# Optimization experiments

Measured on AMD Instinct MI355X. Metric: run time of the kernel, lower is better.

The kernel has to match this reference:

```python
import jax, jax.numpy as jnp
import numpy as np

B, S, D, H = 32, 512, 640, 10
DK = D // H           # 64
NUM_ITER = 3          # capsule routing iterations


def _proj(x, W, b):
    # [B,S,D] @ [D,D]^T -> split heads -> [B,H,S,DK]
    b_, s_, _ = x.shape
    return (x @ W.T + b).reshape(b_, s_, H, DK).transpose(0, 2, 1, 3)


def _squash(t, eps=1e-9):
    sn = jnp.sum(t * t, axis=-1, keepdims=True)
    return (sn / (1.0 + sn)) * t / jnp.sqrt(sn + eps)


def setup_inputs() -> dict:
    key0 = jax.random.key(0)
    ks = jax.random.split(key0, 12)
    s = 1.0 / np.sqrt(D)
    return {
        "query": jax.random.normal(ks[0], (B, S, D), jnp.float32),
        "key": jax.random.normal(ks[1], (B, S, D), jnp.float32),
        "value": jax.random.normal(ks[2], (B, S, D), jnp.float32),
        "mask": jax.random.randint(ks[3], (B, 1, S, S), 0, 2, jnp.int32),
        "adj": jax.random.uniform(ks[4], (B, S, S), jnp.float32),
        "layer": 2,
        "Wq": jax.random.normal(ks[5], (D, D), jnp.float32) * s,
        "bq": jnp.zeros((D,), jnp.float32),
        "Wk": jax.random.normal(ks[6], (D, D), jnp.float32) * s,
        "bk": jnp.zeros((D,), jnp.float32),
        "Wv": jax.random.normal(ks[7], (D, D), jnp.float32) * s,
        "bv": jnp.zeros((D,), jnp.float32),
        # capsule route weights: [num_capsules=1, num_route_nodes=H, DK, D]
        "route_weights": jax.random.normal(ks[8], (1, H, DK, D), jnp.float32) * 0.05,
    }


def reference(query, key, value, mask, adj, layer,
              Wq, bq, Wk, bk, Wv, bv, route_weights):
    q = _proj(query, Wq, bq)   # [B,H,S,DK]
    k = _proj(key, Wk, bk)
    v = _proj(value, Wv, bv)

    # scaled dot-product scores, adjacency + layer-dependent modulation
    scores = jnp.einsum('bhqd,bhkd->bhqk', q, k) / jnp.sqrt(jnp.float32(DK))
    scores = scores + adj[:, None, :, :] / jnp.float32(layer + 1)
    scores = jnp.where(mask == 0, jnp.float32(-1e9), scores)
    p_attn = jax.nn.softmax(scores, axis=-1)            # [B,H,S,S]
    x = jnp.einsum('bhqk,bhkd->bhqd', p_attn, v)        # [B,H,S,DK]

    # [B,H,S,DK] -> [B*S, H, DK]: per-token capsule routing over heads
    x = x.transpose(0, 2, 1, 3).reshape(B * S, H, DK)

    # priors: [num_caps=1, N, H(route nodes), D]
    priors = jnp.einsum('nri,crio->cnro', x, route_weights)
    logits = jnp.zeros(priors.shape[:-1] + (1,), priors.dtype)  # [1,N,H,1]
    out = None
    for i in range(NUM_ITER):
        probs = jax.nn.softmax(logits, axis=2)                  # over route nodes
        out = _squash(jnp.sum(probs * priors, axis=2, keepdims=True))  # [1,N,1,D]
        if i != NUM_ITER - 1:
            logits = logits + jnp.sum(priors * out, axis=-1, keepdims=True)

    return out.reshape(B, S, D)
```

## Files before the change

kernel.cpp:

```cpp
#include <hip/hip_runtime.h>
#include <stdint.h>

#define BB 32
#define SS 512
#define DD 640
#define HH 10
#define DKK 64
#define NTOK (BB*SS)

using f32x4  = __attribute__((ext_vector_type(4))) float;
using bf16x8 = __attribute__((ext_vector_type(8))) __bf16;
using u32x4  = __attribute__((ext_vector_type(4))) unsigned int;
using u32x2  = __attribute__((ext_vector_type(2))) unsigned int;
using u16x4  = __attribute__((ext_vector_type(4))) unsigned short;
using i32x4  = __attribute__((ext_vector_type(4))) int;

__device__ inline unsigned short f2bf(float f){
  union { float f; unsigned int u; } v; v.f=f;
  unsigned int u=v.u;
  u += 0x7FFFu + ((u>>16)&1u);
  return (unsigned short)(u>>16);
}
__device__ inline float bf2f(unsigned short s){
  union { unsigned int u; float f; } v; v.u = ((unsigned int)s)<<16;
  return v.f;
}
__device__ inline unsigned int cvtpk_bf16(float lo, float hi){
  unsigned int r;
  asm volatile("v_cvt_pk_bf16_f32 %0, %1, %2" : "=v"(r) : "v"(lo), "v"(hi));
  return r;
}
__device__ inline void gload_lds16(const unsigned short* g, unsigned short* l){
  __builtin_amdgcn_global_load_lds(
      (const __attribute__((address_space(1))) unsigned int*)g,
      (__attribute__((address_space(3))) unsigned int*)l, 16, 0, 0);
}

__global__ void convert_qkv(const float* __restrict__ q, const float* __restrict__ k,
                            const float* __restrict__ v,
                            unsigned short* __restrict__ xq, unsigned short* __restrict__ xk,
                            unsigned short* __restrict__ xv){
  int i = blockIdx.x*blockDim.x + threadIdx.x;
  const int n4 = (NTOK*DD)/4;
  for (; i < n4; i += gridDim.x*blockDim.x){
    f32x4 a = ((const f32x4*)q)[i];
    f32x4 b = ((const f32x4*)k)[i];
    f32x4 c = ((const f32x4*)v)[i];
    u16x4 ra, rb, rc;
    #pragma unroll
    for (int j=0;j<4;j++){ ra[j]=f2bf(a[j]); rb[j]=f2bf(b[j]); rc[j]=f2bf(c[j]); }
    ((u16x4*)xq)[i]=ra; ((u16x4*)xk)[i]=rb; ((u16x4*)xv)[i]=rc;
  }
}

__global__ void convert_w(const float* __restrict__ wq, const float* __restrict__ wk,
                          const float* __restrict__ wv, const float* __restrict__ rw,
                          unsigned short* __restrict__ bwq, unsigned short* __restrict__ bwk,
                          unsigned short* __restrict__ bwv, unsigned short* __restrict__ brw,
                          unsigned short* __restrict__ brwt){
  int i = blockIdx.x*blockDim.x + threadIdx.x;
  if (i < DD*DD){
    bwq[i]=f2bf(wq[i]); bwk[i]=f2bf(wk[i]); bwv[i]=f2bf(wv[i]);
    unsigned short r = f2bf(rw[i]);
    brw[i]=r;
    int ri = i / DD, o = i % DD;
    brwt[o*DD + ri] = r;
  }
}

__global__ void bias_kernel(const int* __restrict__ mask, const float* __restrict__ adj,
                            const int* __restrict__ layer, unsigned short* __restrict__ biasT){
  float sc = 1.0f/(float)(layer[0]+1);
  int i = blockIdx.x*blockDim.x + threadIdx.x;
  const int n4 = (BB*SS*SS)/4;
  for (; i < n4; i += gridDim.x*blockDim.x){
    i32x4 m = ((const i32x4*)mask)[i];
    f32x4 a = ((const f32x4*)adj)[i];
    u16x4 r;
    #pragma unroll
    for (int j=0;j<4;j++) r[j] = m[j] ? f2bf(a[j]*sc) : f2bf(-1e9f);
    const int e  = i*4;
    const int bb = e >> 18;
    const int qq = (e >> 9) & 511;
    const int kk = e & 511;
    const int idx = (((bb*32 + (qq>>4))*32 + (kk>>4))<<8) + ((qq&15)<<4) + (kk&15);
    *(u16x4*)(biasT + idx) = r;
  }
}

#define BM 128
#define BN 128
#define BK 32

template<typename EPI>
__device__ inline void gemm_body(const unsigned short* __restrict__ A,
                                 const unsigned short* __restrict__ W,
                                 int m0, int n0, EPI&& epi)
{
  __shared__ unsigned short As[2][BM*BK];
  __shared__ unsigned short Ws[2][BN*BK];
  const int tid  = threadIdx.x;
  const int lane = tid & 63;
  const int wave = tid >> 6;
  const int wr   = (wave >> 1) * 64;
  const int wc   = (wave & 1) * 64;
  const int l15  = lane & 15;
  const int g    = lane >> 4;

  f32x4 acc[4][4];
  #pragma unroll
  for (int i=0;i<4;i++)
    #pragma unroll
    for (int j=0;j<4;j++){ f32x4 z = {0.f,0.f,0.f,0.f}; acc[i][j]=z; }

  const int srow  = (lane >> 2);
  const int sunit = (lane & 3) ^ ((lane >> 3) & 3);
  const unsigned short* Ag0 = A + (int64_t)(m0 + wave*32 + srow)*DD + sunit*8;
  const unsigned short* Ag1 = A + (int64_t)(m0 + wave*32 + 16 + srow)*DD + sunit*8;
  const unsigned short* Wg0 = W + (int64_t)(n0 + wave*32 + srow)*DD + sunit*8;
  const unsigned short* Wg1 = W + (int64_t)(n0 + wave*32 + 16 + srow)*DD + sunit*8;

  auto stage = [&](int buf, int k0){
    gload_lds16(Ag0 + k0, As[buf] + wave*1024);
    gload_lds16(Ag1 + k0, As[buf] + wave*1024 + 512);
    gload_lds16(Wg0 + k0, Ws[buf] + wave*1024);
    gload_lds16(Wg1 + k0, Ws[buf] + wave*1024 + 512);
  };

  const int fro = (g ^ ((l15 >> 1) & 3)) * 8;

  stage(0, 0);
  int it = 0;
  for (int k0 = 0; k0 < DD; k0 += BK, it++){
    const int buf = it & 1;
    __syncthreads();
    if (k0 + BK < DD) stage(buf^1, k0 + BK);
    bf16x8 af[4], wf[4];
    #pragma unroll
    for (int m=0;m<4;m++) af[m] = *(const bf16x8*)&As[buf][(wr + m*16 + l15)*BK + fro];
    #pragma unroll
    for (int n=0;n<4;n++) wf[n] = *(const bf16x8*)&Ws[buf][(wc + n*16 + l15)*BK + fro];
    #pragma unroll
    for (int m=0;m<4;m++)
      #pragma unroll
      for (int n=0;n<4;n++)
        acc[m][n] = __builtin_amdgcn_mfma_f32_16x16x32_bf16(af[m], wf[n], acc[m][n], 0,0,0);
  }

  #pragma unroll
  for (int m=0;m<4;m++){
    const int rowbase = m0 + wr + m*16 + g*4;
    #pragma unroll
    for (int n=0;n<4;n++){
      const int col = n0 + wc + n*16 + l15;
      #pragma unroll
      for (int r=0;r<4;r++)
        epi(rowbase + r, col, acc[m][n][r]);
    }
  }
}

__global__ __launch_bounds__(256)
void qkv_gemm(const unsigned short* __restrict__ Xq, const unsigned short* __restrict__ Xk,
              const unsigned short* __restrict__ Xv,
              const unsigned short* __restrict__ bWq, const unsigned short* __restrict__ bWk,
              const unsigned short* __restrict__ bWv,
              const float* __restrict__ bq, const float* __restrict__ bk,
              const float* __restrict__ bv,
              unsigned short* __restrict__ qbuf, unsigned short* __restrict__ kbuf,
              unsigned short* __restrict__ vTbuf)
{
  const int y   = blockIdx.y;
  const int sel = y / 5;
  const int n0  = (y % 5) * BN;
  const int m0  = blockIdx.x * BM;
  const unsigned short* A = sel==0 ? Xq  : sel==1 ? Xk  : Xv;
  const unsigned short* W = sel==0 ? bWq : sel==1 ? bWk : bWv;
  const float*          bb= sel==0 ? bq  : sel==1 ? bk  : bv;
  unsigned short* outp    = sel==0 ? qbuf : kbuf;

  gemm_body(A, W, m0, n0, [&](int row, int col, float v){
    float val = v + bb[col];
    int b=row>>9, s=row&511, h=col>>6, dk=col&63;
    if (sel < 2)
      outp[(((int64_t)(b*HH + h))*SS + s)*DKK + dk] = f2bf(val);
    else
      vTbuf[(((int64_t)(b*HH + h))*DKK + dk)*SS + s] = f2bf(val);
  });
}

__global__ __launch_bounds__(256)
void gemm_nt(const unsigned short* __restrict__ A, const unsigned short* __restrict__ W,
             unsigned short* __restrict__ outp, float scale)
{
  gemm_body(A, W, blockIdx.x*BM, blockIdx.y*BN, [&](int row, int col, float v){
    outp[(int64_t)row*DD + col] = f2bf(v*scale);
  });
}

__global__ __launch_bounds__(256)
void attn_kernel(const unsigned short* __restrict__ qb, const unsigned short* __restrict__ kb,
                 const unsigned short* __restrict__ vT, const unsigned short* __restrict__ biasT,
                 unsigned short* __restrict__ xout)
{
  __shared__ unsigned short SH[20480];
  unsigned short* Kl = SH;
  unsigned short* Vl = SH + 8192;
  char* Pall = (char*)(SH + 16384);

  const int tid  = threadIdx.x;
  const int lane = tid & 63;
  const int wave = tid >> 6;
  const int l15  = lane & 15;
  const int g    = lane >> 4;

  const int orig = blockIdx.x;
  const int wgid = (orig & 7)*320 + (orig >> 3);
  const int h  = wgid % 10;
  const int qt = (wgid / 10) & 7;
  const int b  = wgid / 80;
  const int bh = b*HH + h;

  const unsigned short* Q  = qb + (int64_t)bh*SS*DKK;
  const unsigned short* K  = kb + (int64_t)bh*SS*DKK;
  const unsigned short* V  = vT + (int64_t)bh*DKK*SS;
  const unsigned short* Bt = biasT + (int64_t)((b*32 + qt*4 + wave)*32)*256
                           + l15*16 + g*4;

  const int q0 = qt*64 + wave*16;
  char* Pb = Pall + wave*2048;

  const int srow8 = lane >> 3;
  const int sunit = (lane & 7) ^ (srow8 & 7);

  bf16x8 qf[2];
  #pragma unroll
  for (int ks=0; ks<2; ks++)
    qf[ks] = *(const bf16x8*)(Q + (q0 + l15)*DKK + ks*32 + g*8);

  auto stage = [&](int c, int buf){
    #pragma unroll
    for (int c2=0;c2<2;c2++){
      const int i = wave*2 + c2;
      gload_lds16(K + (int64_t)(c*64 + i*8 + srow8)*DKK + sunit*8,
                  Kl + buf*4096 + i*512);
      gload_lds16(V + (int64_t)(i*8 + srow8)*SS + c*64 + sunit*8,
                  Vl + buf*4096 + i*512);
    }
  };

  float lsum = 0.f;
  f32x4 oacc[4];
  #pragma unroll
  for (int n=0;n<4;n++){ f32x4 z={0.f,0.f,0.f,0.f}; oacc[n]=z; }

  u16x4 bvc[4], bvn[4];
  #pragma unroll
  for (int j=0;j<4;j++) bvc[j] = *(const u16x4*)(Bt + j*256);

  stage(0, 0);
  for (int c = 0; c < 8; c++){
    const int buf = c & 1;
    __syncthreads();
    if (c < 7){
      stage(c+1, buf^1);
      #pragma unroll
      for (int j=0;j<4;j++) bvn[j] = *(const u16x4*)(Bt + ((c+1)*4 + j)*256);
    }

    f32x4 sc[4];
    #pragma unroll
    for (int j=0;j<4;j++){ f32x4 z={0.f,0.f,0.f,0.f}; sc[j]=z; }
    #pragma unroll
    for (int ks=0; ks<2; ks++){
      #pragma unroll
      for (int j=0;j<4;j++){
        bf16x8 kf = *(const bf16x8*)((char*)(Kl + buf*4096)
                     + (j*16 + l15)*128 + (((ks*4+g) ^ (l15&7))*16));
        sc[j] = __builtin_amdgcn_mfma_f32_16x16x32_bf16(kf, qf[ks], sc[j], 0,0,0);
      }
    }
    #pragma unroll
    for (int j=0;j<4;j++){
      float p[4];
      #pragma unroll
      for (int r=0;r<4;r++){
        float s = __builtin_fmaf(sc[j][r], 0.125f, bf2f(bvc[j][r]));
        p[r] = __expf(s - 8.0f);
        lsum += p[r];
      }
      unsigned int w0 = cvtpk_bf16(p[0], p[1]);
      unsigned int w1 = cvtpk_bf16(p[2], p[3]);
      const int kk = j*16 + g*4;
      const int sw = (kk >> 3) ^ (l15 & 7);
      u32x2 w; w[0]=w0; w[1]=w1;
      *(u32x2*)(Pb + l15*128 + sw*16 + (kk&7)*2) = w;
    }
    #pragma unroll
    for (int kt=0; kt<2; kt++){
      bf16x8 pf = *(const bf16x8*)(Pb + l15*128 + (((kt*4+g) ^ (l15&7))*16));
      #pragma unroll
      for (int n=0;n<4;n++){
        bf16x8 vf = *(const bf16x8*)((char*)(Vl + buf*4096)
                     + (n*16 + l15)*128 + (((kt*4+g) ^ (l15&7))*16));
        oacc[n] = __builtin_amdgcn_mfma_f32_16x16x32_bf16(pf, vf, oacc[n], 0,0,0);
      }
    }
    #pragma unroll
    for (int j=0;j<4;j++) bvc[j] = bvn[j];
  }

  lsum += __shfl_xor(lsum, 16);
  lsum += __shfl_xor(lsum, 32);
  const float inv = 1.0f / lsum;
  float invr[4];
  #pragma unroll
  for (int r=0;r<4;r++) invr[r] = __shfl(inv, g*4 + r);

  #pragma unroll
  for (int n=0;n<4;n++){
    const int dk = n*16 + l15;
    #pragma unroll
    for (int r=0;r<4;r++){
      const int qrow = q0 + g*4 + r;
      const int ntok = b*SS + qrow;
      xout[(int64_t)ntok*DD + h*DKK + dk] = f2bf(oacc[n][r] * invr[r]);
    }
  }
}

__global__ void squash_kernel(const unsigned short* __restrict__ sin,
                              unsigned short* __restrict__ bout,
                              float* __restrict__ fout, int final_out)
{
  const int widx = (blockIdx.x*blockDim.x + threadIdx.x) >> 6;
  const int lane = threadIdx.x & 63;
  if (widx >= NTOK) return;
  const unsigned short* row = sin + (int64_t)widx*DD;
  float v[10]; float sn = 0.f;
  #pragma unroll
  for (int i=0;i<10;i++){ v[i] = bf2f(row[i*64 + lane]); sn += v[i]*v[i]; }
  #pragma unroll
  for (int off=1; off<64; off<<=1) sn += __shfl_xor(sn, off);
  const float sc = (sn/(1.0f+sn)) * rsqrtf(sn + 1e-9f);
  if (final_out){
    float* o = fout + (int64_t)widx*DD;
    #pragma unroll
    for (int i=0;i<10;i++) o[i*64+lane] = v[i]*sc;
  } else {
    unsigned short* o = bout + (int64_t)widx*DD;
    #pragma unroll
    for (int i=0;i<10;i++) o[i*64+lane] = f2bf(v[i]*sc);
  }
}

__global__ void route_update(const unsigned short* __restrict__ x,
                             const unsigned short* __restrict__ gbuf,
                             float* __restrict__ logits,
                             unsigned short* __restrict__ xs, int first)
{
  const int widx = (blockIdx.x*blockDim.x + threadIdx.x) >> 6;
  const int lane = threadIdx.x & 63;
  if (widx >= NTOK) return;
  const unsigned short* xr = x + (int64_t)widx*DD;
  const unsigned short* gr = gbuf + (int64_t)widx*DD;
  float xv[10], dv[10];
  #pragma unroll
  for (int i=0;i<10;i++){
    xv[i] = bf2f(xr[i*64+lane]);
    dv[i] = xv[i]*bf2f(gr[i*64+lane]);
  }
  #pragma unroll
  for (int i=0;i<10;i++){
    float v = dv[i];
    #pragma unroll
    for (int off=1; off<64; off<<=1) v += __shfl_xor(v, off);
    dv[i] = v;
  }
  float* lrow = logits + widx*10;
  float lg[10];
  #pragma unroll
  for (int i=0;i<10;i++) lg[i] = first ? dv[i] : (lrow[i] + dv[i]);
  #pragma unroll
  for (int i=0;i<10;i++) if (lane == i) lrow[i] = lg[i];
  float mx = lg[0];
  #pragma unroll
  for (int i=1;i<10;i++) mx = fmaxf(mx, lg[i]);
  float se = 0.f;
  #pragma unroll
  for (int i=0;i<10;i++){ lg[i] = __expf(lg[i]-mx); se += lg[i]; }
  const float inv = 1.0f/se;
  unsigned short* xo = xs + (int64_t)widx*DD;
  #pragma unroll
  for (int i=0;i<10;i++) xo[i*64+lane] = f2bf(xv[i]*lg[i]*inv);
}

extern "C" void kernel_launch(void* const* d_in, const int* in_sizes, int n_in,
                              void* d_out, int out_size, void* d_ws, size_t ws_size,
                              hipStream_t stream)
{
  (void)in_sizes; (void)n_in; (void)out_size; (void)ws_size;
  const float* q    = (const float*)d_in[0];
  const float* k    = (const float*)d_in[1];
  const float* v    = (const float*)d_in[2];
  const int*   mask = (const int*)d_in[3];
  const float* adj  = (const float*)d_in[4];
  const int*   layer= (const int*)d_in[5];
  const float* Wq   = (const float*)d_in[6];
  const float* bq   = (const float*)d_in[7];
  const float* Wk   = (const float*)d_in[8];
  const float* bk   = (const float*)d_in[9];
  const float* Wv   = (const float*)d_in[10];
  const float* bv   = (const float*)d_in[11];
  const float* rw   = (const float*)d_in[12];

  char* ws = (char*)d_ws;
  size_t off = 0;
  auto alloc = [&](size_t sz)->char*{ char* p = ws + off; off += (sz + 255) & ~(size_t)255; return p; };
  const size_t SZX = (size_t)NTOK*DD*2;
  unsigned short* Xq    = (unsigned short*)alloc(SZX);
  unsigned short* Xk    = (unsigned short*)alloc(SZX);
  unsigned short* Xv    = (unsigned short*)alloc(SZX);
  unsigned short* bWq   = (unsigned short*)alloc((size_t)DD*DD*2);
  unsigned short* bWk   = (unsigned short*)alloc((size_t)DD*DD*2);
  unsigned short* bWv   = (unsigned short*)alloc((size_t)DD*DD*2);
  unsigned short* bRW   = (unsigned short*)alloc((size_t)DD*DD*2);
  unsigned short* bRWT  = (unsigned short*)alloc((size_t)DD*DD*2);
  unsigned short* qbuf  = (unsigned short*)alloc(SZX);
  unsigned short* kbuf  = (unsigned short*)alloc(SZX);
  unsigned short* vTbuf = (unsigned short*)alloc(SZX);
  unsigned short* biasb = (unsigned short*)alloc((size_t)BB*SS*SS*2);
  unsigned short* xsb   = (unsigned short*)alloc(SZX);
  float*          logit = (float*)alloc((size_t)NTOK*10*4);
  unsigned short* xout  = Xq;
  unsigned short* outit = Xk;
  unsigned short* gbuf  = Xv;
  unsigned short* sbuf  = qbuf;

  convert_qkv<<<2048,256,0,stream>>>(q,k,v,Xq,Xk,Xv);
  convert_w<<<1600,256,0,stream>>>(Wq,Wk,Wv,rw,bWq,bWk,bWv,bRW,bRWT);
  bias_kernel<<<2048,256,0,stream>>>(mask,adj,layer,biasb);

  dim3 gq(NTOK/BM, 15);
  qkv_gemm<<<gq,256,0,stream>>>(Xq,Xk,Xv,bWq,bWk,bWv,bq,bk,bv,qbuf,kbuf,vTbuf);

  attn_kernel<<<2560,256,0,stream>>>(qbuf,kbuf,vTbuf,biasb,xout);

  dim3 gg(NTOK/BM, DD/BN);
  gemm_nt<<<gg,256,0,stream>>>(xout,bRWT,sbuf,0.1f);
  squash_kernel<<<4096,256,0,stream>>>(sbuf,outit,nullptr,0);
  gemm_nt<<<gg,256,0,stream>>>(outit,bRW,gbuf,1.0f);
  route_update<<<4096,256,0,stream>>>(xout,gbuf,logit,xsb,1);
  gemm_nt<<<gg,256,0,stream>>>(xsb,bRWT,sbuf,1.0f);
  squash_kernel<<<4096,256,0,stream>>>(sbuf,outit,nullptr,0);
  gemm_nt<<<gg,256,0,stream>>>(outit,bRW,gbuf,1.0f);
  route_update<<<4096,256,0,stream>>>(xout,gbuf,logit,xsb,0);
  gemm_nt<<<gg,256,0,stream>>>(xsb,bRWT,sbuf,1.0f);
  squash_kernel<<<4096,256,0,stream>>>(sbuf,nullptr,(float*)d_out,1);
}
```

Measured before the change: 348.4 us.

## Replace iterative capsule routing GEMMs with per-token Gram matrix routing

Routing is reformulated algebraically. Each token gets a 10x10 Gram matrix of its per-head priors, computed with MFMA in a new gram_kernel, and all three routing iterations then run on that small matrix in shared memory. A single final GEMM applies the weighted input to the route weights and writes fp32 output directly. This replaces five full GEMMs plus five elementwise kernels, and drops the non-transposed weight copy and the logits buffer. The cost is that the Gram kernel still computes the priors internally and reads RWT from global memory with no reuse across blocks, and accuracy now depends on the Gram and final GEMM arithmetic.

```diff
diff --git a/kernel.cpp b/kernel.cpp
--- a/kernel.cpp
+++ b/kernel.cpp
@@ -56,13 +56,11 @@
 __global__ void convert_w(const float* __restrict__ wq, const float* __restrict__ wk,
                           const float* __restrict__ wv, const float* __restrict__ rw,
                           unsigned short* __restrict__ bwq, unsigned short* __restrict__ bwk,
-                          unsigned short* __restrict__ bwv, unsigned short* __restrict__ brw,
-                          unsigned short* __restrict__ brwt){
+                          unsigned short* __restrict__ bwv, unsigned short* __restrict__ brwt){
   int i = blockIdx.x*blockDim.x + threadIdx.x;
   if (i < DD*DD){
     bwq[i]=f2bf(wq[i]); bwk[i]=f2bf(wk[i]); bwv[i]=f2bf(wv[i]);
     unsigned short r = f2bf(rw[i]);
-    brw[i]=r;
     int ri = i / DD, o = i % DD;
     brwt[o*DD + ri] = r;
   }
@@ -190,11 +188,11 @@
 }
 
 __global__ __launch_bounds__(256)
-void gemm_nt(const unsigned short* __restrict__ A, const unsigned short* __restrict__ W,
-             unsigned short* __restrict__ outp, float scale)
+void final_gemm(const unsigned short* __restrict__ A, const unsigned short* __restrict__ W,
+                float* __restrict__ outp)
 {
   gemm_body(A, W, blockIdx.x*BM, blockIdx.y*BN, [&](int row, int col, float v){
-    outp[(int64_t)row*DD + col] = f2bf(v*scale);
+    outp[(int64_t)row*DD + col] = v;
   });
 }
 
@@ -329,70 +327,139 @@
   }
 }
 
-__global__ void squash_kernel(const unsigned short* __restrict__ sin,
-                              unsigned short* __restrict__ bout,
-                              float* __restrict__ fout, int final_out)
+__global__ __launch_bounds__(256)
+void gram_kernel(const unsigned short* __restrict__ x,
+                 const unsigned short* __restrict__ RWT,
+                 unsigned short* __restrict__ xw)
 {
-  const int widx = (blockIdx.x*blockDim.x + threadIdx.x) >> 6;
-  const int lane = threadIdx.x & 63;
-  if (widx >= NTOK) return;
-  const unsigned short* row = sin + (int64_t)widx*DD;
-  float v[10]; float sn = 0.f;
-  #pragma unroll
-  for (int i=0;i<10;i++){ v[i] = bf2f(row[i*64 + lane]); sn += v[i]*v[i]; }
-  #pragma unroll
-  for (int off=1; off<64; off<<=1) sn += __shfl_xor(sn, off);
-  const float sc = (sn/(1.0f+sn)) * rsqrtf(sn + 1e-9f);
-  if (final_out){
-    float* o = fout + (int64_t)widx*DD;
-    #pragma unroll
-    for (int i=0;i<10;i++) o[i*64+lane] = v[i]*sc;
-  } else {
-    unsigned short* o = bout + (int64_t)widx*DD;
-    #pragma unroll
-    for (int i=0;i<10;i++) o[i*64+lane] = f2bf(v[i]*sc);
-  }
-}
-
-__global__ void route_update(const unsigned short* __restrict__ x,
-                             const unsigned short* __restrict__ gbuf,
-                             float* __restrict__ logits,
-                             unsigned short* __restrict__ xs, int first)
-{
-  const int widx = (blockIdx.x*blockDim.x + threadIdx.x) >> 6;
-  const int lane = threadIdx.x & 63;
-  if (widx >= NTOK) return;
-  const unsigned short* xr = x + (int64_t)widx*DD;
-  const unsigned short* gr = gbuf + (int64_t)widx*DD;
-  float xv[10], dv[10];
-  #pragma unroll
-  for (int i=0;i<10;i++){
-    xv[i] = bf2f(xr[i*64+lane]);
-    dv[i] = xv[i]*bf2f(gr[i*64+lane]);
-  }
-  #pragma unroll
-  for (int i=0;i<10;i++){
-    float v = dv[i];
-    #pragma unroll
-    for (int off=1; off<64; off<<=1) v += __shfl_xor(v, off);
-    dv[i] = v;
-  }
-  float* lrow = logits + widx*10;
-  float lg[10];
-  #pragma unroll
-  for (int i=0;i<10;i++) lg[i] = first ? dv[i] : (lrow[i] + dv[i]);
-  #pragma unroll
-  for (int i=0;i<10;i++) if (lane == i) lrow[i] = lg[i];
-  float mx = lg[0];
-  #pragma unroll
-  for (int i=1;i<10;i++) mx = fmaxf(mx, lg[i]);
-  float se = 0.f;
-  #pragma unroll
-  for (int i=0;i<10;i++){ lg[i] = __expf(lg[i]-mx); se += lg[i]; }
-  const float inv = 1.0f/se;
-  unsigned short* xo = xs + (int64_t)widx*DD;
-  #pragma unroll
-  for (int i=0;i<10;i++) xo[i*64+lane] = f2bf(xv[i]*lg[i]*inv);
+  __shared__ unsigned short Xl[16*664];
+  __shared__ float Gp[4][16][56];
+  __shared__ float Gfin[16][56];
+  __shared__ float Pr[16][10];
+  __shared__ float Dm[16][10];
+  __shared__ float Lg[16][10];
+  __shared__ float wl[16][10];
+
+  const int tid  = threadIdx.x;
+  const int lane = tid & 63;
+  const int wave = tid >> 6;
+  const int l15  = lane & 15;
+  const int g    = lane >> 4;
+  const int tok0 = blockIdx.x * 16;
+
+  #pragma unroll
+  for (int rd=0; rd<5; rd++){
+    const int idx = rd*2048 + tid*8;
+    const int tk  = idx / 640;
+    const int cl  = idx - tk*640;
+    u32x4 vv = *(const u32x4*)(x + (int64_t)tok0*640 + idx);
+    *(u32x4*)&Xl[tk*664 + cl] = vv;
+  }
+  __syncthreads();
+
+  float Gacc[55];
+  #pragma unroll
+  for (int p=0;p<55;p++) Gacc[p]=0.f;
+
+  for (int ot=0; ot<10; ot++){
+    const int o0 = (wave*10 + ot)*16;
+    f32x4 P[10];
+    #pragma unroll
+    for (int r=0;r<10;r++){ f32x4 z={0.f,0.f,0.f,0.f}; P[r]=z; }
+    #pragma unroll
+    for (int r=0;r<10;r++){
+      #pragma unroll
+      for (int ks=0;ks<2;ks++){
+        bf16x8 af = *(const bf16x8*)&RWT[(int64_t)(o0+l15)*DD + r*64 + ks*32 + g*8];
+        bf16x8 xf = *(const bf16x8*)&Xl[l15*664 + r*64 + ks*32 + g*8];
+        P[r] = __builtin_amdgcn_mfma_f32_16x16x32_bf16(af, xf, P[r], 0,0,0);
+      }
+    }
+    #pragma unroll
+    for (int r=0;r<10;r++)
+      #pragma unroll
+      for (int rp=r; rp<10; rp++){
+        const int T = r*10 - r*(r-1)/2 + (rp-r);
+        Gacc[T] += P[r][0]*P[rp][0] + P[r][1]*P[rp][1]
+                 + P[r][2]*P[rp][2] + P[r][3]*P[rp][3];
+      }
+  }
+  #pragma unroll
+  for (int p=0;p<55;p++){
+    Gacc[p] += __shfl_xor(Gacc[p], 16);
+    Gacc[p] += __shfl_xor(Gacc[p], 32);
+  }
+  if (lane < 16){
+    #pragma unroll
+    for (int p=0;p<55;p++) Gp[wave][lane][p] = Gacc[p];
+  }
+  __syncthreads();
+  {
+    const int gtok = tid & 15;
+    for (int p = tid>>4; p < 55; p += 16)
+      Gfin[gtok][p] = Gp[0][gtok][p]+Gp[1][gtok][p]+Gp[2][gtok][p]+Gp[3][gtok][p];
+  }
+  __syncthreads();
+
+  const int tok = tid >> 4, rp = tid & 15;
+  const bool act = rp < 10;
+  float grow[10]; float Lr = 0.f;
+  if (act){
+    #pragma unroll
+    for (int r=0;r<10;r++){
+      const int lo = r < rp ? r : rp, hi = r < rp ? rp : r;
+      grow[r] = Gfin[tok][lo*10 - lo*(lo-1)/2 + (hi-lo)];
+    }
+    Pr[tok][rp] = 0.1f;
+  }
+  __syncthreads();
+  for (int it=0; it<3; it++){
+    float d = 0.f;
+    if (act){
+      #pragma unroll
+      for (int r=0;r<10;r++) d += grow[r]*Pr[tok][r];
+      Dm[tok][rp] = d;
+    }
+    __syncthreads();
+    if (act){
+      float sn = 0.f;
+      #pragma unroll
+      for (int r=0;r<10;r++) sn += Dm[tok][r]*Pr[tok][r];
+      const float sc = (sn/(1.f+sn))*rsqrtf(sn+1e-9f);
+      if (it < 2){ Lr += sc*d; Lg[tok][rp] = Lr; }
+      else        wl[tok][rp] = sc*Pr[tok][rp];
+    }
+    __syncthreads();
+    if (it < 2){
+      if (act){
+        float mx = Lg[tok][0];
+        #pragma unroll
+        for (int r=1;r<10;r++) mx = fmaxf(mx, Lg[tok][r]);
+        float se = 0.f;
+        #pragma unroll
+        for (int r=0;r<10;r++) se += __expf(Lg[tok][r]-mx);
+        Pr[tok][rp] = __expf(Lr-mx)/se;
+      }
+      __syncthreads();
+    }
+  }
+
+  {
+    const int tk = tid >> 4, seg = tid & 15;
+    #pragma unroll
+    for (int j=0;j<5;j++){
+      const int c = seg*40 + j*8;
+      const float w = wl[tk][c>>6];
+      u16x4 a = *(const u16x4*)&Xl[tk*664 + c];
+      u16x4 b = *(const u16x4*)&Xl[tk*664 + c + 4];
+      u32x4 o;
+      o[0] = cvtpk_bf16(bf2f(a[0])*w, bf2f(a[1])*w);
+      o[1] = cvtpk_bf16(bf2f(a[2])*w, bf2f(a[3])*w);
+      o[2] = cvtpk_bf16(bf2f(b[0])*w, bf2f(b[1])*w);
+      o[3] = cvtpk_bf16(bf2f(b[2])*w, bf2f(b[3])*w);
+      *(u32x4*)&xw[(int64_t)(tok0+tk)*DD + c] = o;
+    }
+  }
 }
 
 extern "C" void kernel_launch(void* const* d_in, const int* in_sizes, int n_in,
@@ -424,21 +491,16 @@
   unsigned short* bWq   = (unsigned short*)alloc((size_t)DD*DD*2);
   unsigned short* bWk   = (unsigned short*)alloc((size_t)DD*DD*2);
   unsigned short* bWv   = (unsigned short*)alloc((size_t)DD*DD*2);
-  unsigned short* bRW   = (unsigned short*)alloc((size_t)DD*DD*2);
   unsigned short* bRWT  = (unsigned short*)alloc((size_t)DD*DD*2);
   unsigned short* qbuf  = (unsigned short*)alloc(SZX);
   unsigned short* kbuf  = (unsigned short*)alloc(SZX);
   unsigned short* vTbuf = (unsigned short*)alloc(SZX);
   unsigned short* biasb = (unsigned short*)alloc((size_t)BB*SS*SS*2);
-  unsigned short* xsb   = (unsigned short*)alloc(SZX);
-  float*          logit = (float*)alloc((size_t)NTOK*10*4);
   unsigned short* xout  = Xq;
-  unsigned short* outit = Xk;
-  unsigned short* gbuf  = Xv;
-  unsigned short* sbuf  = qbuf;
+  unsigned short* xw    = Xk;
 
   convert_qkv<<<2048,256,0,stream>>>(q,k,v,Xq,Xk,Xv);
-  convert_w<<<1600,256,0,stream>>>(Wq,Wk,Wv,rw,bWq,bWk,bWv,bRW,bRWT);
+  convert_w<<<1600,256,0,stream>>>(Wq,Wk,Wv,rw,bWq,bWk,bWv,bRWT);
   bias_kernel<<<2048,256,0,stream>>>(mask,adj,layer,biasb);
 
   dim3 gq(NTOK/BM, 15);
@@ -446,15 +508,8 @@
 
   attn_kernel<<<2560,256,0,stream>>>(qbuf,kbuf,vTbuf,biasb,xout);
 
-  dim3 gg(NTOK/BM, DD/BN);
-  gemm_nt<<<gg,256,0,stream>>>(xout,bRWT,sbuf,0.1f);
-  squash_kernel<<<4096,256,0,stream>>>(sbuf,outit,nullptr,0);
-  gemm_nt<<<gg,256,0,stream>>>(outit,bRW,gbuf,1.0f);
-  route_update<<<4096,256,0,stream>>>(xout,gbuf,logit,xsb,1);
-  gemm_nt<<<gg,256,0,stream>>>(xsb,bRWT,sbuf,1.0f);
-  squash_kernel<<<4096,256,0,stream>>>(sbuf,outit,nullptr,0);
-  gemm_nt<<<gg,256,0,stream>>>(outit,bRW,gbuf,1.0f);
-  route_update<<<4096,256,0,stream>>>(xout,gbuf,logit,xsb,0);
-  gemm_nt<<<gg,256,0,stream>>>(xsb,bRWT,sbuf,1.0f);
-  squash_kernel<<<4096,256,0,stream>>>(sbuf,nullptr,(float*)d_out,1);
-}
+  gram_kernel<<<NTOK/16,256,0,stream>>>(xout,bRWT,xw);
+
+  dim3 gf(NTOK/BM, DD/BN);
+  final_gemm<<<gf,256,0,stream>>>(xw,bRWT,(float*)d_out);
+}
```

After: 325.1 us. -6.7%, faster.
